# Kernel optimization log

Hardware: AMD Instinct MI355X
Metric: run time of the kernel (lower is better)

Reference implementation:

```python
import jax, jax.numpy as jnp
import numpy as np

B, S, D = 2, 2048, 1024
H, HD = 16, 64          # num_heads, head_dim = dim_feedforward // num_heads
ROPE_BASE = 10000.0


def _apply_rope(t):
    # t: [b, h, s, hd] -> RoPE applied over last dim, positions = token index
    b, h, s, hd = t.shape
    theta = 1.0 / (ROPE_BASE ** (jnp.arange(0, hd, 2, dtype=jnp.float32) / hd))  # [hd/2]
    ang = jnp.arange(s, dtype=jnp.float32)[:, None] * theta[None, :]             # [s, hd/2]
    cos, sin = jnp.cos(ang), jnp.sin(ang)
    tr = t.reshape(b, h, s, hd // 2, 2)
    t0, t1 = tr[..., 0], tr[..., 1]
    o0 = t0 * cos - t1 * sin
    o1 = t1 * cos + t0 * sin
    return jnp.stack([o0, o1], axis=-1).reshape(b, h, s, hd)


def setup_inputs() -> dict:
    key = jax.random.key(0)
    ks = jax.random.split(key, 8)
    x = jax.random.normal(ks[0], (B, S, D), dtype=jnp.float32)
    wq = jax.random.normal(ks[1], (D, H * HD), dtype=jnp.float32) * 0.02
    wk = jax.random.normal(ks[2], (D, H * HD), dtype=jnp.float32) * 0.02
    wv = jax.random.normal(ks[3], (D, H * HD), dtype=jnp.float32) * 0.02
    bq = jax.random.normal(ks[4], (H * HD,), dtype=jnp.float32) * 0.02
    bk = jax.random.normal(ks[5], (H * HD,), dtype=jnp.float32) * 0.02
    bv = jax.random.normal(ks[6], (H * HD,), dtype=jnp.float32) * 0.02
    # trailing padding per batch; valid_len large enough that every causal+history
    # window contains at least one unpadded key (valid_len > S - max_history)
    valid_len = jax.random.randint(ks[7], (B,), S - 256, S + 1)
    key_padding_mask = (jnp.arange(S)[None, :] >= valid_len[:, None]).astype(jnp.int32)
    return {"x": x, "wq": wq, "bq": bq, "wk": wk, "bk": bk, "wv": wv, "bv": bv,
            "key_padding_mask": key_padding_mask, "max_history_len": 512}


def reference(x, wq, bq, wk, bk, wv, bv, key_padding_mask, max_history_len):
    b, s, d = x.shape
    scale = HD ** (-0.5)
    q = (x @ wq + bq).reshape(b, s, H, HD).transpose(0, 2, 1, 3)  # [b,h,s,hd]
    k = (x @ wk + bk).reshape(b, s, H, HD).transpose(0, 2, 1, 3)
    v = (x @ wv + bv).reshape(b, s, H, HD).transpose(0, 2, 1, 3)
    q = _apply_rope(q)
    k = _apply_rope(k)
    scores = jnp.einsum('bhqd,bhkd->bhqk', q, k) * scale          # [b,h,s,s]
    i = jnp.arange(s)[:, None]
    j = jnp.arange(s)[None, :]
    band = (j <= i) & ((i - j) <= (max_history_len - 1))          # causal + history
    allowed = band[None, None, :, :] & (key_padding_mask == 0)[:, None, None, :]
    scores = jnp.where(allowed, scores, -jnp.inf)
    attn = jax.nn.softmax(scores, axis=-1)
    out = jnp.einsum('bhqk,bhkd->bhqd', attn, v)                  # [b,h,s,hd]
    return out.transpose(0, 2, 1, 3).reshape(b, s, H * HD)
```

## Files before the change

### kernel.cpp

```cpp
#include <hip/hip_runtime.h>
#include <hip/hip_bf16.h>
#include <stdint.h>


typedef __attribute__((ext_vector_type(8))) short bf16x8;
typedef __attribute__((ext_vector_type(4))) short bf16x4;
typedef __attribute__((ext_vector_type(4))) float f32x4;

#define DEV __device__ __forceinline__

DEV ushort f2b(float f) {
  union { float f; uint32_t u; } v; v.f = f;
  uint32_t r = v.u + 0x7FFFu + ((v.u >> 16) & 1u);
  return (ushort)(r >> 16);
}
DEV float b2f(ushort u) {
  union { uint32_t u; float f; } v; v.u = ((uint32_t)u) << 16;
  return v.f;
}
DEV uint cvt_pk_bf16(float lo, float hi) {
  uint r;
  asm("v_cvt_pk_bf16_f32 %0, %1, %2" : "=v"(r) : "v"(lo), "v"(hi));
  return r;
}
DEV float fast_exp2(float x) {
#if __has_builtin(__builtin_amdgcn_exp2f)
  return __builtin_amdgcn_exp2f(x);
#else
  return exp2f(x);
#endif
}

DEV void gload_lds16(const void* g, void* l) {
  __builtin_amdgcn_global_load_lds((const __attribute__((address_space(1))) void*)g,
                                   (__attribute__((address_space(3))) void*)l,
                                   16, 0, 0);
}

__global__ __launch_bounds__(256) void prep_kernel(
    const float* __restrict__ x, ushort* __restrict__ xb,
    const float* __restrict__ wq, const float* __restrict__ wk,
    const float* __restrict__ wv, ushort* __restrict__ wt,
    float2* __restrict__ tab) {
  int bid = blockIdx.x, tid = threadIdx.x;
  if (bid < 4096) {
    int t = bid * 256 + tid;
    float4 v = ((const float4*)x)[t];
    bf16x4 o;
    o[0] = (short)f2b(v.x); o[1] = (short)f2b(v.y);
    o[2] = (short)f2b(v.z); o[3] = (short)f2b(v.w);
    *(bf16x4*)&xb[(size_t)t * 4] = o;
  } else if (bid < 4352) {
    int t = (bid - 4096) * 256 + tid;
    int i = t & 31, s = t >> 5;
    float theta = powf(10000.0f, -(float)i / 32.0f);
    float ang = (float)s * theta;
    tab[t] = make_float2(cosf(ang), sinf(ang));
  } else {
    __shared__ float tile[32][33];
    int rem = bid - 4352;
    int which = rem >> 10, t2 = rem & 1023;
    int n0 = (t2 & 31) * 32, k0 = (t2 >> 5) * 32;
    const float* w = which == 0 ? wq : (which == 1 ? wk : wv);
    int r = tid >> 3, c4 = (tid & 7) * 4;
    float4 v = *(const float4*)&w[(size_t)(k0 + r) * 1024 + n0 + c4];
    tile[r][c4] = v.x; tile[r][c4 + 1] = v.y;
    tile[r][c4 + 2] = v.z; tile[r][c4 + 3] = v.w;
    __syncthreads();
    bf16x4 o;
#pragma unroll
    for (int i = 0; i < 4; ++i) o[i] = (short)f2b(tile[c4 + i][r]);
    *(bf16x4*)&wt[((size_t)(which * 1024 + n0 + r)) * 1024 + k0 + c4] = o;
  }
}

__global__ __launch_bounds__(512, 2) void qkv_gemm_kernel(
    const ushort* __restrict__ A, const ushort* __restrict__ Bt,
    const float* __restrict__ bq, const float* __restrict__ bk,
    const float* __restrict__ bv, const float2* __restrict__ tab,
    ushort* __restrict__ qb, ushort* __restrict__ kb, ushort* __restrict__ vt) {
  const int K = 1024;
  __shared__ alignas(16) ushort sA[2][256 * 64];
  __shared__ alignas(16) ushort sB[2][192 * 64];

  int tid = threadIdx.x;
  int lane = tid & 63;
  int lhi = lane >> 4, llo = lane & 15;
  int wid = tid >> 6;
  int wr = wid >> 2, wc = wid & 3;

  int id = blockIdx.x;
  int wg = (id & 7) * 32 + (id >> 3);
  int bm = wg >> 4, bn = wg & 15;

  const ushort* Abase = A + (size_t)bm * 256 * K;
  const ushort* Bbase = Bt + (size_t)bn * 192 * K;

  f32x4 acc[8][3];
#pragma unroll
  for (int i = 0; i < 8; ++i)
#pragma unroll
    for (int j = 0; j < 3; ++j) acc[i][j] = (f32x4){0.f, 0.f, 0.f, 0.f};

  auto stage = [&](int kt, int bb) {
    int k0 = kt * 64;
#pragma unroll
    for (int c = 0; c < 4; ++c) {
      int idx = c * 512 + tid;
      int row = idx >> 3, gslot = (idx & 7) ^ (row & 7);
      gload_lds16(Abase + (size_t)row * K + k0 + gslot * 8, &sA[bb][(idx & ~63) * 8]);
    }
#pragma unroll
    for (int c = 0; c < 3; ++c) {
      int idx = c * 512 + tid;
      int row = idx >> 3, gslot = (idx & 7) ^ (row & 7);
      gload_lds16(Bbase + (size_t)row * K + k0 + gslot * 8, &sB[bb][(idx & ~63) * 8]);
    }
  };

  stage(0, 0); stage(1, 1);

  for (int kt = 0; kt < 16; ++kt) {
    if (kt < 15) asm volatile("s_waitcnt vmcnt(7)" ::: "memory");
    else         asm volatile("s_waitcnt vmcnt(0)" ::: "memory");
    __builtin_amdgcn_sched_barrier(0);
    __builtin_amdgcn_s_barrier();
    __builtin_amdgcn_sched_barrier(0);

    int buf = kt & 1;
    const ushort* pA = sA[buf];
    const ushort* pB = sB[buf];

    bf16x8 bfr[3][2], af[4][2];
#pragma unroll
    for (int nf = 0; nf < 3; ++nf) {
      int r = wc * 48 + nf * 16 + llo;
#pragma unroll
      for (int ks = 0; ks < 2; ++ks)
        bfr[nf][ks] = *(const bf16x8*)&pB[r * 64 + (((ks * 4 + lhi) ^ (r & 7)) * 8)];
    }
#pragma unroll
    for (int mf = 0; mf < 4; ++mf) {
      int r = wr * 128 + mf * 16 + llo;
#pragma unroll
      for (int ks = 0; ks < 2; ++ks)
        af[mf][ks] = *(const bf16x8*)&pA[r * 64 + (((ks * 4 + lhi) ^ (r & 7)) * 8)];
    }
    __builtin_amdgcn_s_setprio(1);
#pragma unroll
    for (int mf = 0; mf < 4; ++mf)
#pragma unroll
      for (int nf = 0; nf < 3; ++nf)
#pragma unroll
        for (int ks = 0; ks < 2; ++ks)
          acc[mf][nf] = __builtin_amdgcn_mfma_f32_16x16x32_bf16(bfr[nf][ks], af[mf][ks], acc[mf][nf], 0, 0, 0);
    __builtin_amdgcn_s_setprio(0);
    __builtin_amdgcn_sched_barrier(0);
    __builtin_amdgcn_s_barrier();
    __builtin_amdgcn_sched_barrier(0);

#pragma unroll
    for (int mf = 0; mf < 4; ++mf) {
      int r = wr * 128 + (4 + mf) * 16 + llo;
#pragma unroll
      for (int ks = 0; ks < 2; ++ks)
        af[mf][ks] = *(const bf16x8*)&pA[r * 64 + (((ks * 4 + lhi) ^ (r & 7)) * 8)];
    }
    asm volatile("s_waitcnt lgkmcnt(0)" ::: "memory");
    __builtin_amdgcn_sched_barrier(0);
    __builtin_amdgcn_s_barrier();
    __builtin_amdgcn_sched_barrier(0);
    if (kt + 2 < 16) stage(kt + 2, buf);
    __builtin_amdgcn_s_setprio(1);
#pragma unroll
    for (int mf = 0; mf < 4; ++mf)
#pragma unroll
      for (int nf = 0; nf < 3; ++nf)
#pragma unroll
        for (int ks = 0; ks < 2; ++ks)
          acc[4 + mf][nf] = __builtin_amdgcn_mfma_f32_16x16x32_bf16(bfr[nf][ks], af[mf][ks], acc[4 + mf][nf], 0, 0, 0);
    __builtin_amdgcn_s_setprio(0);
    __builtin_amdgcn_sched_barrier(0);
  }

  const float SCL = 0.18033688011112042f;
#pragma unroll
  for (int mf = 0; mf < 8; ++mf) {
    int m = bm * 256 + wr * 128 + mf * 16 + llo;
    int s = m & 2047, bidx = m >> 11;
#pragma unroll
    for (int nf = 0; nf < 3; ++nf) {
      int nbase = bn * 192 + wc * 48 + nf * 16;
      int n0 = nbase + lhi * 4;
      f32x4 a = acc[mf][nf];
      if (nbase < 1024) {
        float4 cs = *(const float4*)&tab[s * 32 + ((n0 & 63) >> 1)];
        float4 bb = *(const float4*)&bq[n0];
        float t0 = a[0] + bb.x, t1 = a[1] + bb.y;
        float t2 = a[2] + bb.z, t3 = a[3] + bb.w;
        uint2 ov;
        ov.x = cvt_pk_bf16((t0 * cs.x - t1 * cs.y) * SCL, (t1 * cs.x + t0 * cs.y) * SCL);
        ov.y = cvt_pk_bf16((t2 * cs.z - t3 * cs.w) * SCL, (t3 * cs.z + t2 * cs.w) * SCL);
        int h = n0 >> 6;
        *(uint2*)&qb[((size_t)(bidx * 16 + h) * 2048 + s) * 64 + (n0 & 63)] = ov;
      } else if (nbase < 2048) {
        float4 cs = *(const float4*)&tab[s * 32 + ((n0 & 63) >> 1)];
        float4 bb = *(const float4*)&bk[n0 - 1024];
        float t0 = a[0] + bb.x, t1 = a[1] + bb.y;
        float t2 = a[2] + bb.z, t3 = a[3] + bb.w;
        uint2 ov;
        ov.x = cvt_pk_bf16(t0 * cs.x - t1 * cs.y, t1 * cs.x + t0 * cs.y);
        ov.y = cvt_pk_bf16(t2 * cs.z - t3 * cs.w, t3 * cs.z + t2 * cs.w);
        int h = (n0 >> 6) & 15;
        *(uint2*)&kb[((size_t)(bidx * 16 + h) * 2048 + s) * 64 + (n0 & 63)] = ov;
      } else {
        float4 bb = *(const float4*)&bv[n0 - 2048];
        int hd_g = n0 - 2048;
        int h = hd_g >> 6, hd = hd_g & 63;
        size_t vb = ((size_t)(bidx * 16 + h) * 64 + hd) * 2048 + s;
        vt[vb]        = f2b(a[0] + bb.x);
        vt[vb + 2048] = f2b(a[1] + bb.y);
        vt[vb + 4096] = f2b(a[2] + bb.z);
        vt[vb + 6144] = f2b(a[3] + bb.w);
      }
    }
  }
}

__global__ __launch_bounds__(512) void attn_kernel(
    const ushort* __restrict__ qb, const ushort* __restrict__ kb,
    const ushort* __restrict__ vt, const int* __restrict__ kmask,
    const int* __restrict__ whist, float* __restrict__ out) {
  __shared__ alignas(16) ushort sK[128 * 64];
  __shared__ alignas(16) ushort sV[64 * 136];
  __shared__ alignas(16) uint   sPd[8][16 * 68];

  int tid = threadIdx.x;
  int lane = tid & 63, wid = tid >> 6;
  int lhi = lane >> 4, llo = lane & 15;

  int id = blockIdx.x;
  int xcd = id & 7, sub = id >> 3;
  int bh = xcd * 4 + (sub >> 4);
  int qtile = sub & 15;
  int b = bh >> 4;
  int q0 = qtile * 128;
  int qw0 = q0 + wid * 16;
  int W = *whist;

  const ushort* qptr = qb + (size_t)bh * 2048 * 64;
  const ushort* kptr = kb + (size_t)bh * 2048 * 64;
  const ushort* vptr = vt + (size_t)bh * 64 * 2048;
  const int* mrow = kmask + b * 2048;

  bf16x8 qf0, qf1;
  {
    size_t base = (size_t)(qw0 + llo) * 64 + lhi * 8;
    qf0 = *(const bf16x8*)&qptr[base];
    qf1 = *(const bf16x8*)&qptr[base + 32];
  }

  float l_ = 0.f;
  f32x4 o[4];
#pragma unroll
  for (int nf = 0; nf < 4; ++nf) o[nf] = (f32x4){0.f, 0.f, 0.f, 0.f};

  int lo = q0 - (W - 1); if (lo < 0) lo = 0;
  int jt0 = lo & ~127;
  int nt = ((q0 + 128) - jt0) >> 7;

  bf16x8 kreg[2], vreg[2];
  int mreg0, mreg1;
  int krow = tid >> 2, kslot2 = (tid & 3) * 2;
  int vrow = tid >> 3, vslot2 = (tid & 7) * 2;

  auto load_tile = [&](int jt) {
    kreg[0] = *(const bf16x8*)&kptr[(size_t)(jt + krow) * 64 + kslot2 * 8];
    kreg[1] = *(const bf16x8*)&kptr[(size_t)(jt + krow) * 64 + (kslot2 + 1) * 8];
    vreg[0] = *(const bf16x8*)&vptr[(size_t)vrow * 2048 + jt + vslot2 * 8];
    vreg[1] = *(const bf16x8*)&vptr[(size_t)vrow * 2048 + jt + (vslot2 + 1) * 8];
    mreg0 = mrow[jt + lane];
    mreg1 = mrow[jt + 64 + lane];
  };

  load_tile(jt0);
  for (int it = 0; it < nt; ++it) {
    int jt = jt0 + it * 128;
    __syncthreads();
    *(bf16x8*)&sK[krow * 64 + ((kslot2 ^ (krow & 7)) * 8)] = kreg[0];
    *(bf16x8*)&sK[krow * 64 + (((kslot2 + 1) ^ (krow & 7)) * 8)] = kreg[1];
    *(bf16x8*)&sV[vrow * 136 + vslot2 * 8] = vreg[0];
    *(bf16x8*)&sV[vrow * 136 + (vslot2 + 1) * 8] = vreg[1];
    unsigned long long pm0 = __ballot(mreg0 != 0);
    unsigned long long pm1 = __ballot(mreg1 != 0);
    if (it + 1 < nt) load_tile(jt + 128);
    __syncthreads();

    bool active = (jt <= qw0 + 15) && (jt + 127 >= qw0 - W + 1);
    if (active) {
      f32x4 sc[8];
#pragma unroll
      for (int kb8 = 0; kb8 < 8; ++kb8) sc[kb8] = (f32x4){0.f, 0.f, 0.f, 0.f};
      __builtin_amdgcn_s_setprio(1);
#pragma unroll
      for (int ks = 0; ks < 2; ++ks) {
        bf16x8 qq = ks ? qf1 : qf0;
#pragma unroll
        for (int kb8 = 0; kb8 < 8; ++kb8) {
          int r = kb8 * 16 + llo;
          bf16x8 kf = *(const bf16x8*)&sK[r * 64 + (((ks * 4 + lhi) ^ (r & 7)) * 8)];
          sc[kb8] = __builtin_amdgcn_mfma_f32_16x16x32_bf16(kf, qq, sc[kb8], 0, 0, 0);
        }
      }
      __builtin_amdgcn_s_setprio(0);

      bool fastp = (jt + 127 <= qw0) && (jt >= qw0 + 16 - W) &&
                   (pm0 == 0ull) && (pm1 == 0ull);
      if (!fastp) {
        int qi = qw0 + llo;
#pragma unroll
        for (int kb8 = 0; kb8 < 8; ++kb8) {
          uint nib = (uint)((kb8 < 4 ? pm0 : pm1) >> ((kb8 & 3) * 16 + lhi * 4)) & 0xFu;
#pragma unroll
          for (int j = 0; j < 4; ++j) {
            int key = jt + kb8 * 16 + lhi * 4 + j;
            bool k_ok = (key <= qi) && (qi - key < W) && !((nib >> j) & 1u);
            sc[kb8][j] = k_ok ? sc[kb8][j] : -1e30f;
          }
        }
      }

#pragma unroll
      for (int kb8 = 0; kb8 < 8; ++kb8)
#pragma unroll
        for (int j = 0; j < 4; ++j) sc[kb8][j] = fast_exp2(sc[kb8][j]);

      uint* prow = &sPd[wid][llo * 68];
#pragma unroll
      for (int kb8 = 0; kb8 < 8; ++kb8) {
        uint2 d;
        d.x = cvt_pk_bf16(sc[kb8][0], sc[kb8][1]);
        d.y = cvt_pk_bf16(sc[kb8][2], sc[kb8][3]);
        *(uint2*)&prow[kb8 * 8 + lhi * 2] = d;
      }

      float sm[8];
#pragma unroll
      for (int kb8 = 0; kb8 < 8; ++kb8)
        sm[kb8] = (sc[kb8][0] + sc[kb8][1]) + (sc[kb8][2] + sc[kb8][3]);
      float ps = ((sm[0] + sm[1]) + (sm[2] + sm[3])) + ((sm[4] + sm[5]) + (sm[6] + sm[7]));
      ps += __shfl_xor(ps, 16);
      ps += __shfl_xor(ps, 32);
      l_ += ps;

      bf16x8 pf[4];
#pragma unroll
      for (int ksb = 0; ksb < 4; ++ksb)
        pf[ksb] = *(const bf16x8*)&sPd[wid][llo * 68 + ksb * 16 + lhi * 4];

      __builtin_amdgcn_s_setprio(1);
#pragma unroll
      for (int nf = 0; nf < 4; ++nf) {
#pragma unroll
        for (int ksb = 0; ksb < 4; ++ksb) {
          bf16x8 vf = *(const bf16x8*)&sV[(nf * 16 + llo) * 136 + ksb * 32 + lhi * 8];
          o[nf] = __builtin_amdgcn_mfma_f32_16x16x32_bf16(vf, pf[ksb], o[nf], 0, 0, 0);
        }
      }
      __builtin_amdgcn_s_setprio(0);
    }
  }

  float inv = 1.f / l_;
  int qi = qw0 + llo;
  size_t obase = ((size_t)b * 2048 + qi) * 1024 + (bh & 15) * 64 + lhi * 4;
#pragma unroll
  for (int nf = 0; nf < 4; ++nf) {
    float4 st = make_float4(o[nf][0] * inv, o[nf][1] * inv, o[nf][2] * inv, o[nf][3] * inv);
    *(float4*)&out[obase + nf * 16] = st;
  }
}

extern "C" void kernel_launch(void* const* d_in, const int* in_sizes, int n_in,
                              void* d_out, int out_size, void* d_ws, size_t ws_size,
                              hipStream_t stream) {
  const float* x  = (const float*)d_in[0];
  const float* wq = (const float*)d_in[1];
  const float* bq = (const float*)d_in[2];
  const float* wk = (const float*)d_in[3];
  const float* bk = (const float*)d_in[4];
  const float* wv = (const float*)d_in[5];
  const float* bv = (const float*)d_in[6];
  const int* kmask = (const int*)d_in[7];
  const int* whist = (const int*)d_in[8];
  float* out = (float*)d_out;

  char* ws = (char*)d_ws;
  ushort* xb  = (ushort*)(ws);
  ushort* wt  = (ushort*)(ws + (8ull  << 20));
  ushort* qb  = (ushort*)(ws + (14ull << 20));
  ushort* kb  = (ushort*)(ws + (22ull << 20));
  ushort* vt  = (ushort*)(ws + (30ull << 20));
  float2* tab = (float2*)(ws + (38ull << 20));

  prep_kernel<<<7424, 256, 0, stream>>>(x, xb, wq, wk, wv, wt, tab);
  qkv_gemm_kernel<<<256, 512, 0, stream>>>(xb, wt, bq, bk, bv, tab, qb, kb, vt);
  attn_kernel<<<512, 512, 0, stream>>>(qb, kb, vt, kmask, whist, out);
}
```

Before: 69.08 us.

## Software-pipeline LDS fragment reads in QKV GEMM and defer softmax row-sum reduction

```diff
diff --git a/kernel.cpp b/kernel.cpp
--- a/kernel.cpp
+++ b/kernel.cpp
@@ -118,20 +118,9 @@
     }
   };
 
-  stage(0, 0); stage(1, 1);
-
-  for (int kt = 0; kt < 16; ++kt) {
-    if (kt < 15) asm volatile("s_waitcnt vmcnt(7)" ::: "memory");
-    else         asm volatile("s_waitcnt vmcnt(0)" ::: "memory");
-    __builtin_amdgcn_sched_barrier(0);
-    __builtin_amdgcn_s_barrier();
-    __builtin_amdgcn_sched_barrier(0);
-
-    int buf = kt & 1;
-    const ushort* pA = sA[buf];
-    const ushort* pB = sB[buf];
-
-    bf16x8 bfr[3][2], af[4][2];
+  bf16x8 bfr[3][2], af0[4][2], af1[4][2];
+
+  auto readG0 = [&](const ushort* pA, const ushort* pB) {
 #pragma unroll
     for (int nf = 0; nf < 3; ++nf) {
       int r = wc * 48 + nf * 16 + llo;
@@ -144,8 +133,31 @@
       int r = wr * 128 + mf * 16 + llo;
 #pragma unroll
       for (int ks = 0; ks < 2; ++ks)
-        af[mf][ks] = *(const bf16x8*)&pA[r * 64 + (((ks * 4 + lhi) ^ (r & 7)) * 8)];
-    }
+        af0[mf][ks] = *(const bf16x8*)&pA[r * 64 + (((ks * 4 + lhi) ^ (r & 7)) * 8)];
+    }
+  };
+  auto readG1 = [&](const ushort* pA) {
+#pragma unroll
+    for (int mf = 0; mf < 4; ++mf) {
+      int r = wr * 128 + (4 + mf) * 16 + llo;
+#pragma unroll
+      for (int ks = 0; ks < 2; ++ks)
+        af1[mf][ks] = *(const bf16x8*)&pA[r * 64 + (((ks * 4 + lhi) ^ (r & 7)) * 8)];
+    }
+  };
+
+  stage(0, 0); stage(1, 1);
+  asm volatile("s_waitcnt vmcnt(7)" ::: "memory");
+  __builtin_amdgcn_sched_barrier(0);
+  __builtin_amdgcn_s_barrier();
+  __builtin_amdgcn_sched_barrier(0);
+  readG0(sA[0], sB[0]);
+
+  for (int kt = 0; kt < 16; ++kt) {
+    int buf = kt & 1;
+    readG1(sA[buf]);
+    asm volatile("s_waitcnt lgkmcnt(8)" ::: "memory");
+    __builtin_amdgcn_sched_barrier(0);
     __builtin_amdgcn_s_setprio(1);
 #pragma unroll
     for (int mf = 0; mf < 4; ++mf)
@@ -153,34 +165,31 @@
       for (int nf = 0; nf < 3; ++nf)
 #pragma unroll
         for (int ks = 0; ks < 2; ++ks)
-          acc[mf][nf] = __builtin_amdgcn_mfma_f32_16x16x32_bf16(bfr[nf][ks], af[mf][ks], acc[mf][nf], 0, 0, 0);
+          acc[mf][nf] = __builtin_amdgcn_mfma_f32_16x16x32_bf16(bfr[nf][ks], af0[mf][ks], acc[mf][nf], 0, 0, 0);
+    __builtin_amdgcn_s_setprio(0);
+    asm volatile("s_waitcnt lgkmcnt(0)" ::: "memory");
+    __builtin_amdgcn_sched_barrier(0);
+    __builtin_amdgcn_s_setprio(1);
+#pragma unroll
+    for (int mf = 0; mf < 4; ++mf)
+#pragma unroll
+      for (int nf = 0; nf < 3; ++nf)
+#pragma unroll
+        for (int ks = 0; ks < 2; ++ks)
+          acc[4 + mf][nf] = __builtin_amdgcn_mfma_f32_16x16x32_bf16(bfr[nf][ks], af1[mf][ks], acc[4 + mf][nf], 0, 0, 0);
     __builtin_amdgcn_s_setprio(0);
     __builtin_amdgcn_sched_barrier(0);
     __builtin_amdgcn_s_barrier();
     __builtin_amdgcn_sched_barrier(0);
-
-#pragma unroll
-    for (int mf = 0; mf < 4; ++mf) {
-      int r = wr * 128 + (4 + mf) * 16 + llo;
-#pragma unroll
-      for (int ks = 0; ks < 2; ++ks)
-        af[mf][ks] = *(const bf16x8*)&pA[r * 64 + (((ks * 4 + lhi) ^ (r & 7)) * 8)];
-    }
-    asm volatile("s_waitcnt lgkmcnt(0)" ::: "memory");
-    __builtin_amdgcn_sched_barrier(0);
-    __builtin_amdgcn_s_barrier();
-    __builtin_amdgcn_sched_barrier(0);
     if (kt + 2 < 16) stage(kt + 2, buf);
-    __builtin_amdgcn_s_setprio(1);
-#pragma unroll
-    for (int mf = 0; mf < 4; ++mf)
-#pragma unroll
-      for (int nf = 0; nf < 3; ++nf)
-#pragma unroll
-        for (int ks = 0; ks < 2; ++ks)
-          acc[4 + mf][nf] = __builtin_amdgcn_mfma_f32_16x16x32_bf16(bfr[nf][ks], af[mf][ks], acc[4 + mf][nf], 0, 0, 0);
-    __builtin_amdgcn_s_setprio(0);
-    __builtin_amdgcn_sched_barrier(0);
+    if (kt + 1 < 16) {
+      if (kt + 2 < 16) asm volatile("s_waitcnt vmcnt(7)" ::: "memory");
+      else             asm volatile("s_waitcnt vmcnt(0)" ::: "memory");
+      __builtin_amdgcn_sched_barrier(0);
+      __builtin_amdgcn_s_barrier();
+      __builtin_amdgcn_sched_barrier(0);
+      readG0(sA[buf ^ 1], sB[buf ^ 1]);
+    }
   }
 
   const float SCL = 0.18033688011112042f;
@@ -348,10 +357,7 @@
 #pragma unroll
       for (int kb8 = 0; kb8 < 8; ++kb8)
         sm[kb8] = (sc[kb8][0] + sc[kb8][1]) + (sc[kb8][2] + sc[kb8][3]);
-      float ps = ((sm[0] + sm[1]) + (sm[2] + sm[3])) + ((sm[4] + sm[5]) + (sm[6] + sm[7]));
-      ps += __shfl_xor(ps, 16);
-      ps += __shfl_xor(ps, 32);
-      l_ += ps;
+      l_ += ((sm[0] + sm[1]) + (sm[2] + sm[3])) + ((sm[4] + sm[5]) + (sm[6] + sm[7]));
 
       bf16x8 pf[4];
 #pragma unroll
@@ -371,6 +377,8 @@
     }
   }
 
+  l_ += __shfl_xor(l_, 16);
+  l_ += __shfl_xor(l_, 32);
   float inv = 1.f / l_;
   int qi = qw0 + llo;
   size_t obase = ((size_t)b * 2048 + qi) * 1024 + (bh & 15) * 64 + lhi * 4;
```

New measurement: 70.99 us. 1.03x slower.
